# Performance work log

Hardware: AMD Instinct MI355X
Metric: run time of the kernel (lower is better)

Reference implementation:

```python
import jax, jax.numpy as jnp
import numpy as np
from jax import lax

NUM_HEADS = 8
EPS = 1e-12  # torch F.normalize eps


def setup_inputs() -> dict:
    key = jax.random.key(0)
    ks = jax.random.split(key, 5)
    dim = 192
    b, h, w = 8, 128, 128
    return {
        "x": jax.random.normal(ks[0], (b, dim, h, w), jnp.float32),
        "w_qkv": jax.random.normal(ks[1], (3 * dim, dim, 1, 1), jnp.float32) * (1.0 / np.sqrt(dim)),
        "w_dw": jax.random.normal(ks[2], (3 * dim, 1, 3, 3), jnp.float32) * (1.0 / 3.0),
        "w_proj": jax.random.normal(ks[3], (dim, dim, 1, 1), jnp.float32) * (1.0 / np.sqrt(dim)),
        "temperature": jnp.ones((NUM_HEADS, 1, 1), jnp.float32),
    }


def _l2norm(t):
    n = jnp.sqrt(jnp.sum(t * t, axis=-1, keepdims=True))
    return t / jnp.maximum(n, EPS)


def reference(x, w_qkv, w_dw, w_proj, temperature):
    b, c, h, w = x.shape
    # 1x1 conv to 3*dim channels
    qkv = jnp.einsum('bchw,oc->bohw', x, w_qkv[:, :, 0, 0])
    # depthwise 3x3 conv, dilation=2, padding=2, groups=3*dim
    qkv = lax.conv_general_dilated(
        qkv, w_dw, window_strides=(1, 1), padding=((2, 2), (2, 2)),
        rhs_dilation=(2, 2), feature_group_count=3 * c,
        dimension_numbers=('NCHW', 'OIHW', 'NCHW'))
    q, k, v = jnp.split(qkv, 3, axis=1)
    ch = c // NUM_HEADS
    def heads(t):  # b (head ch) h w -> b head ch (h w)
        return t.reshape(b, NUM_HEADS, ch, h * w)
    q, k, v = heads(q), heads(k), heads(v)
    q = _l2norm(q)
    k = _l2norm(k)
    attn = jnp.einsum('bhcn,bhdn->bhcd', q, k) * temperature  # (b, head, ch, ch)
    attn = jax.nn.softmax(attn, axis=-1)
    out = jnp.einsum('bhcd,bhdn->bhcn', attn, v)
    out = out.reshape(b, c, h, w)
    out = jnp.einsum('bchw,oc->bohw', out, w_proj[:, :, 0, 0])
    return out
```

## Files before the change

### kernel.cpp

```cpp
#include <hip/hip_runtime.h>


#define DIM 192
#define NH 8
#define CH 24
#define IH 128
#define IW 128
#define NPIX (IH*IW)
#define BATCH 8
#define QKVC (3*DIM)
#define PAD 200
#define TPAD 136
#define SPAD 264

typedef unsigned short u16;
typedef short bf16x8 __attribute__((ext_vector_type(8)));
typedef float f32x4 __attribute__((ext_vector_type(4)));

__device__ __forceinline__ float b2f(u16 u){
    unsigned v = ((unsigned)u) << 16;
    return __builtin_bit_cast(float, v);
}
__device__ __forceinline__ u16 f2b(float f){
    unsigned u = __builtin_bit_cast(unsigned, f);
    u += 0x7fffu + ((u >> 16) & 1u);
    return (u16)(u >> 16);
}

__device__ __forceinline__ void conv_row8(const u16* __restrict__ rp, int px0,
        float w0, float w1, float w2, float* o_){
    float f[12];
    if(px0 > 0){
        unsigned u = *(const unsigned*)(rp + px0 - 2);
        f[0] = b2f((u16)u); f[1] = b2f((u16)(u >> 16));
    } else { f[0] = 0.f; f[1] = 0.f; }
    bf16x8 v = *(const bf16x8*)(rp + px0);
    #pragma unroll
    for(int j=0;j<8;j++) f[2+j] = b2f((u16)v[j]);
    if(px0 < 120){
        unsigned u = *(const unsigned*)(rp + px0 + 8);
        f[10] = b2f((u16)u); f[11] = b2f((u16)(u >> 16));
    } else { f[10] = 0.f; f[11] = 0.f; }
    #pragma unroll
    for(int i=0;i<8;i++) o_[i] += w0*f[i] + w1*f[i+2] + w2*f[i+4];
}

__global__ __launch_bounds__(256) void k1_qkv(const float* __restrict__ x,
        const float* __restrict__ wqkv, u16* __restrict__ qkv_pre){
    __shared__ __align__(16) u16 Xl[128*PAD];
    __shared__ __align__(16) u16 Wl[64*PAD];
    const int tid = threadIdx.x;
    const int pt = blockIdx.x, b = blockIdx.y;
    const int p0 = pt*128;
    {
        const int px = tid & 127, half = tid >> 7;
        const float* xb = x + (size_t)b*DIM*NPIX + p0 + px;
        for(int cg = 0; cg < 12; cg++){
            int cb = half*96 + cg*8;
            bf16x8 v;
            #pragma unroll
            for(int j=0;j<8;j++) v[j] = (short)f2b(xb[(size_t)(cb+j)*NPIX]);
            *(bf16x8*)&Xl[px*PAD + cb] = v;
        }
    }
    const int lane = tid & 63, w = tid >> 6;
    const int r = lane & 15, quad = lane >> 4;
    const int mbase = (w & 1)*32, nbase = (w >> 1)*64;
    u16* Tl = Wl;
    for(int ot = 0; ot < 9; ot++){
        const int obase = ot*64;
        for(int i = tid; i < 64*24; i += 256){
            int o = i/24, k8 = (i%24)*8;
            const float* wp = wqkv + (size_t)(obase+o)*DIM + k8;
            bf16x8 v;
            #pragma unroll
            for(int j=0;j<8;j++) v[j] = (short)f2b(wp[j]);
            *(bf16x8*)&Wl[o*PAD + k8] = v;
        }
        __syncthreads();
        f32x4 acc[8];
        { f32x4 z = {0.f,0.f,0.f,0.f}; for(int i=0;i<8;i++) acc[i]=z; }
        #pragma unroll
        for(int kk = 0; kk < 6; kk++){
            const int k0 = kk*32 + quad*8;
            bf16x8 a0 = *(const bf16x8*)&Wl[(mbase + r)*PAD + k0];
            bf16x8 a1 = *(const bf16x8*)&Wl[(mbase + 16 + r)*PAD + k0];
            #pragma unroll
            for(int ni=0; ni<4; ni++){
                bf16x8 bb = *(const bf16x8*)&Xl[(nbase + ni*16 + r)*PAD + k0];
                acc[ni*2+0] = __builtin_amdgcn_mfma_f32_16x16x32_bf16(a0, bb, acc[ni*2+0], 0,0,0);
                acc[ni*2+1] = __builtin_amdgcn_mfma_f32_16x16x32_bf16(a1, bb, acc[ni*2+1], 0,0,0);
            }
        }
        __syncthreads();
        #pragma unroll
        for(int ni=0; ni<4; ni++)
            #pragma unroll
            for(int mi=0; mi<2; mi++){
                int o_loc = mbase + mi*16 + quad*4;
                int p_loc = nbase + ni*16 + r;
                #pragma unroll
                for(int t=0;t<4;t++)
                    Tl[(o_loc+t)*TPAD + p_loc] = f2b(acc[ni*2+mi][t]);
            }
        __syncthreads();
        u16* op = qkv_pre + ((size_t)b*QKVC + obase)*NPIX + p0;
        for(int it = 0; it < 4; it++){
            int idx = tid + it*256;
            int o = idx >> 4, oct = idx & 15;
            bf16x8 v = *(const bf16x8*)&Tl[o*TPAD + oct*8];
            *(bf16x8*)&op[(size_t)o*NPIX + oct*8] = v;
        }
        __syncthreads();
    }
}

__global__ __launch_bounds__(256) void k2_gram(const u16* __restrict__ qkv_pre,
        const float* __restrict__ wdw, float* __restrict__ G){
    __shared__ __align__(16) u16 Sl[48*SPAD];
    const int tid = threadIdx.x;
    const int pc = blockIdx.x, h = blockIdx.y, b = blockIdx.z;
    const int lane = tid & 63, w = tid >> 6;
    const int r = lane & 15, quad = lane >> 4;
    f32x4 acc[6];
    { f32x4 z = {0.f,0.f,0.f,0.f}; for(int i=0;i<6;i++) acc[i]=z; }
    for(int chunk = 0; chunk < 2; chunk++){
        if(chunk) __syncthreads();
        for(int it = 0; it < 6; it++){
            int t = tid + it*256;
            int c48 = t >> 5, oct = t & 31;
            int isK = (c48 >= CH);
            int c = isK ? (c48 - CH) : c48;
            int ch = (isK ? DIM : 0) + h*CH + c;
            const u16* base = qkv_pre + ((size_t)b*QKVC + ch)*NPIX;
            const float* wv = wdw + ch*9;
            int py = pc*4 + chunk*2 + (oct >> 4);
            int px0 = (oct & 15)*8;
            float o_[8];
            #pragma unroll
            for(int i=0;i<8;i++) o_[i]=0.f;
            #pragma unroll
            for(int ky=0;ky<3;ky++){
                int ry = py + 2*ky - 2;
                if(ry < 0 || ry >= IH) continue;
                conv_row8(base + ry*IW, px0, wv[ky*3], wv[ky*3+1], wv[ky*3+2], o_);
            }
            bf16x8 v;
            #pragma unroll
            for(int i=0;i<8;i++) v[i] = (short)f2b(o_[i]);
            *(bf16x8*)&Sl[c48*SPAD + oct*8] = v;
        }
        __syncthreads();
        #pragma unroll
        for(int kk = 0; kk < 2; kk++){
            const int k0 = w*64 + kk*32 + quad*8;
            bf16x8 f0 = *(const bf16x8*)&Sl[(     r)*SPAD + k0];
            bf16x8 f1 = *(const bf16x8*)&Sl[(16 + r)*SPAD + k0];
            bf16x8 f2 = *(const bf16x8*)&Sl[(32 + r)*SPAD + k0];
            acc[0] = __builtin_amdgcn_mfma_f32_16x16x32_bf16(f0, f0, acc[0], 0,0,0);
            acc[1] = __builtin_amdgcn_mfma_f32_16x16x32_bf16(f0, f1, acc[1], 0,0,0);
            acc[2] = __builtin_amdgcn_mfma_f32_16x16x32_bf16(f0, f2, acc[2], 0,0,0);
            acc[3] = __builtin_amdgcn_mfma_f32_16x16x32_bf16(f1, f1, acc[3], 0,0,0);
            acc[4] = __builtin_amdgcn_mfma_f32_16x16x32_bf16(f1, f2, acc[4], 0,0,0);
            acc[5] = __builtin_amdgcn_mfma_f32_16x16x32_bf16(f2, f2, acc[5], 0,0,0);
        }
    }
    __syncthreads();
    float* R = (float*)Sl;
    #pragma unroll
    for(int tile=0; tile<6; tile++)
        *(f32x4*)&R[(w*6 + tile)*256 + lane*4] = acc[tile];
    __syncthreads();
    float* Gb = G + (size_t)(b*NH + h)*48*48;
    #pragma unroll
    for(int i=0; i<6; i++){
        int idx = tid + i*256;
        int tile = idx >> 8, rem = idx & 255;
        int ln = rem >> 2, t = rem & 3;
        float s = R[idx] + R[1536 + idx] + R[2*1536 + idx] + R[3*1536 + idx];
        int ti = (tile<3) ? 0 : ((tile<5) ? 1 : 2);
        int tj = (tile<3) ? tile : ((tile<5) ? (tile-2) : 2);
        int c = ti*16 + (ln >> 4)*4 + t;
        int d = tj*16 + (ln & 15);
        atomicAdd(&Gb[c*48 + d], s);
    }
}

__global__ __launch_bounds__(256) void k4_vconv(u16* __restrict__ qkv_pre,
        const float* __restrict__ wdw){
    const int tid = threadIdx.x;
    const int oct = tid & 15, pyl = tid >> 4;
    const int band = blockIdx.x, cp = blockIdx.y, b = blockIdx.z;
    const int py = band*16 + pyl, px0 = oct*8;
    #pragma unroll
    for(int j=0;j<2;j++){
        int ch = cp*2 + j;
        const u16* base = qkv_pre + ((size_t)b*QKVC + 2*DIM + ch)*NPIX;
        const float* wv = wdw + (2*DIM + ch)*9;
        float o_[8];
        #pragma unroll
        for(int i=0;i<8;i++) o_[i]=0.f;
        #pragma unroll
        for(int ky=0;ky<3;ky++){
            int ry = py + 2*ky - 2;
            if(ry < 0 || ry >= IH) continue;
            conv_row8(base + ry*IW, px0, wv[ky*3], wv[ky*3+1], wv[ky*3+2], o_);
        }
        bf16x8 v;
        #pragma unroll
        for(int i=0;i<8;i++) v[i] = (short)f2b(o_[i]);
        *(bf16x8*)&qkv_pre[((size_t)b*QKVC + ch)*NPIX + py*IW + px0] = v;
    }
}

__global__ __launch_bounds__(256) void k3_attn(const float* __restrict__ G,
        const float* __restrict__ temp, const float* __restrict__ wproj,
        float* __restrict__ M){
    __shared__ float attn[NH][CH][CH];
    __shared__ float nq[DIM], nk[DIM];
    const int b = blockIdx.x, tid = threadIdx.x;
    const float* Gb = G + (size_t)b*NH*48*48;
    if(tid < DIM){
        int h = tid / CH, c = tid % CH;
        const float* g = Gb + (size_t)h*48*48;
        nq[tid] = fmaxf(sqrtf(g[c*48 + c]), 1e-12f);
        nk[tid] = fmaxf(sqrtf(g[(CH+c)*48 + (CH+c)]), 1e-12f);
    }
    __syncthreads();
    if(tid < DIM){
        int h = tid / CH, c = tid % CH;
        float t = temp[h];
        const float* g = Gb + (size_t)h*48*48 + c*48 + CH;
        float row[CH];
        float mx = -1e30f;
        #pragma unroll
        for(int d=0; d<CH; d++){
            float v = g[d] / (nq[tid]*nk[h*CH+d]) * t;
            row[d]=v; mx = fmaxf(mx,v);
        }
        float sum=0.f;
        #pragma unroll
        for(int d=0;d<CH;d++){ row[d]=expf(row[d]-mx); sum+=row[d]; }
        float inv = 1.f/sum;
        #pragma unroll
        for(int d=0;d<CH;d++) attn[h][c][d] = row[d]*inv;
    }
    __syncthreads();
    float* Mb = M + (size_t)b*DIM*DIM;
    for(int i = tid; i < DIM*DIM; i += 256){
        int o = i / DIM, hd = i % DIM;
        int h = hd / CH, d = hd % CH;
        float s = 0.f;
        #pragma unroll
        for(int c=0;c<CH;c++)
            s += wproj[o*DIM + h*CH + c] * attn[h][c][d];
        Mb[i] = s;
    }
}

__global__ __launch_bounds__(256) void k5_out(const u16* __restrict__ qkv_pre,
        const float* __restrict__ M, float* __restrict__ out){
    __shared__ __align__(16) u16 vl[128*PAD];
    __shared__ __align__(16) u16 Ml[64*PAD];
    const int tid = threadIdx.x;
    const int py = blockIdx.x, b = blockIdx.y;
    const int p0 = py*IW;
    {
        const int px = tid & 127, half = tid >> 7;
        const u16* vb = qkv_pre + (size_t)b*QKVC*NPIX + p0 + px;
        for(int cg = 0; cg < 12; cg++){
            int cb = half*96 + cg*8;
            bf16x8 v;
            #pragma unroll
            for(int j=0;j<8;j++) v[j] = (short)vb[(size_t)(cb+j)*NPIX];
            *(bf16x8*)&vl[px*PAD + cb] = v;
        }
    }
    const int lane = tid & 63, w = tid >> 6;
    const int r = lane & 15, quad = lane >> 4;
    const int mbase = (w & 1)*32, nbase = (w >> 1)*64;
    for(int ot = 0; ot < 3; ot++){
        const int obase = ot*64;
        for(int i = tid; i < 64*24; i += 256){
            int o = i/24, k8 = (i%24)*8;
            const float* mp = M + ((size_t)b*DIM + obase + o)*DIM + k8;
            bf16x8 v;
            #pragma unroll
            for(int j=0;j<8;j++) v[j] = (short)f2b(mp[j]);
            *(bf16x8*)&Ml[o*PAD + k8] = v;
        }
        __syncthreads();
        f32x4 acc[8];
        { f32x4 z = {0.f,0.f,0.f,0.f}; for(int i=0;i<8;i++) acc[i]=z; }
        #pragma unroll
        for(int kk = 0; kk < 6; kk++){
            const int k0 = kk*32 + quad*8;
            bf16x8 a0 = *(const bf16x8*)&Ml[(mbase + r)*PAD + k0];
            bf16x8 a1 = *(const bf16x8*)&Ml[(mbase + 16 + r)*PAD + k0];
            #pragma unroll
            for(int ni=0; ni<4; ni++){
                bf16x8 bb = *(const bf16x8*)&vl[(nbase + ni*16 + r)*PAD + k0];
                acc[ni*2+0] = __builtin_amdgcn_mfma_f32_16x16x32_bf16(a0, bb, acc[ni*2+0], 0,0,0);
                acc[ni*2+1] = __builtin_amdgcn_mfma_f32_16x16x32_bf16(a1, bb, acc[ni*2+1], 0,0,0);
            }
        }
        float* op = out + ((size_t)b*DIM + obase)*NPIX + p0;
        #pragma unroll
        for(int ni=0; ni<4; ni++)
            #pragma unroll
            for(int mi=0; mi<2; mi++){
                int o_loc = mbase + mi*16 + quad*4;
                int p_loc = nbase + ni*16 + r;
                #pragma unroll
                for(int t=0;t<4;t++)
                    op[(size_t)(o_loc+t)*NPIX + p_loc] = acc[ni*2+mi][t];
            }
        __syncthreads();
    }
}

extern "C" void kernel_launch(void* const* d_in, const int* in_sizes, int n_in,
                              void* d_out, int out_size, void* d_ws, size_t ws_size,
                              hipStream_t stream){
    const float* x     = (const float*)d_in[0];
    const float* wqkv  = (const float*)d_in[1];
    const float* wdw   = (const float*)d_in[2];
    const float* wproj = (const float*)d_in[3];
    const float* temp  = (const float*)d_in[4];
    float* out = (float*)d_out;

    char* ws = (char*)d_ws;
    u16* qkv_pre = (u16*)ws;
    size_t off = (size_t)BATCH*QKVC*NPIX*sizeof(u16);
    float* G   = (float*)(ws + off); off += (size_t)BATCH*NH*48*48*4;
    float* M   = (float*)(ws + off); off += (size_t)BATCH*DIM*DIM*4;

    hipMemsetAsync(G, 0, (size_t)BATCH*NH*48*48*sizeof(float), stream);

    k1_qkv <<<dim3(128, BATCH), 256, 0, stream>>>(x, wqkv, qkv_pre);
    k2_gram<<<dim3(32, NH, BATCH), 256, 0, stream>>>(qkv_pre, wdw, G);
    k4_vconv<<<dim3(8, 96, BATCH), 256, 0, stream>>>(qkv_pre, wdw);
    k3_attn<<<BATCH, 256, 0, stream>>>(G, temp, wproj, M);
    k5_out <<<dim3(128, BATCH), 256, 0, stream>>>(qkv_pre, M, out);
}
```

Before: 447.1 us.

## Pre-convert weights to bf16 and read MFMA A operands directly from global

Adds a small kernel that converts the qkv weight to bf16 once, and makes the attention kernel emit the fused projection matrix M in bf16. The k1 and k5 GEMM kernels then load weight fragments straight from global/L2 instead of staging them through shared memory each tile, which removes several __syncthreads per output tile and the per-block fp32-to-bf16 conversion. k1 also swaps the MFMA operand order so each lane holds four consecutive pixels, letting it store packed bf16 results directly to global without the LDS transpose. The costs are scattered global loads for the A operands and narrower 8-byte stores, plus one extra kernel launch.

```diff
diff --git a/kernel.cpp b/kernel.cpp
--- a/kernel.cpp
+++ b/kernel.cpp
@@ -10,7 +10,6 @@
 #define BATCH 8
 #define QKVC (3*DIM)
 #define PAD 200
-#define TPAD 136
 #define SPAD 264
 
 typedef unsigned short u16;
@@ -45,10 +44,18 @@
     for(int i=0;i<8;i++) o_[i] += w0*f[i] + w1*f[i+2] + w2*f[i+4];
 }
 
+__global__ __launch_bounds__(256) void k0_wcvt(const float* __restrict__ wqkv,
+        u16* __restrict__ wb){
+    int i = (blockIdx.x*256 + threadIdx.x)*4;
+    f32x4 v = *(const f32x4*)&wqkv[i];
+    unsigned lo = ((unsigned)f2b(v[1]) << 16) | f2b(v[0]);
+    unsigned hi = ((unsigned)f2b(v[3]) << 16) | f2b(v[2]);
+    *(uint2*)&wb[i] = make_uint2(lo, hi);
+}
+
 __global__ __launch_bounds__(256) void k1_qkv(const float* __restrict__ x,
-        const float* __restrict__ wqkv, u16* __restrict__ qkv_pre){
+        const u16* __restrict__ wb, u16* __restrict__ qkv_pre){
     __shared__ __align__(16) u16 Xl[128*PAD];
-    __shared__ __align__(16) u16 Wl[64*PAD];
     const int tid = threadIdx.x;
     const int pt = blockIdx.x, b = blockIdx.y;
     const int p0 = pt*128;
@@ -63,55 +70,40 @@
             *(bf16x8*)&Xl[px*PAD + cb] = v;
         }
     }
+    __syncthreads();
     const int lane = tid & 63, w = tid >> 6;
     const int r = lane & 15, quad = lane >> 4;
     const int mbase = (w & 1)*32, nbase = (w >> 1)*64;
-    u16* Tl = Wl;
+    u16* op = qkv_pre + (size_t)b*QKVC*NPIX + p0;
     for(int ot = 0; ot < 9; ot++){
         const int obase = ot*64;
-        for(int i = tid; i < 64*24; i += 256){
-            int o = i/24, k8 = (i%24)*8;
-            const float* wp = wqkv + (size_t)(obase+o)*DIM + k8;
-            bf16x8 v;
-            #pragma unroll
-            for(int j=0;j<8;j++) v[j] = (short)f2b(wp[j]);
-            *(bf16x8*)&Wl[o*PAD + k8] = v;
-        }
-        __syncthreads();
         f32x4 acc[8];
         { f32x4 z = {0.f,0.f,0.f,0.f}; for(int i=0;i<8;i++) acc[i]=z; }
+        const u16* w0p = wb + (size_t)(obase + mbase + r)*DIM;
+        const u16* w1p = w0p + 16*DIM;
         #pragma unroll
         for(int kk = 0; kk < 6; kk++){
             const int k0 = kk*32 + quad*8;
-            bf16x8 a0 = *(const bf16x8*)&Wl[(mbase + r)*PAD + k0];
-            bf16x8 a1 = *(const bf16x8*)&Wl[(mbase + 16 + r)*PAD + k0];
+            bf16x8 a0 = *(const bf16x8*)&w0p[k0];
+            bf16x8 a1 = *(const bf16x8*)&w1p[k0];
             #pragma unroll
             for(int ni=0; ni<4; ni++){
                 bf16x8 bb = *(const bf16x8*)&Xl[(nbase + ni*16 + r)*PAD + k0];
-                acc[ni*2+0] = __builtin_amdgcn_mfma_f32_16x16x32_bf16(a0, bb, acc[ni*2+0], 0,0,0);
-                acc[ni*2+1] = __builtin_amdgcn_mfma_f32_16x16x32_bf16(a1, bb, acc[ni*2+1], 0,0,0);
-            }
-        }
-        __syncthreads();
+                acc[ni*2+0] = __builtin_amdgcn_mfma_f32_16x16x32_bf16(bb, a0, acc[ni*2+0], 0,0,0);
+                acc[ni*2+1] = __builtin_amdgcn_mfma_f32_16x16x32_bf16(bb, a1, acc[ni*2+1], 0,0,0);
+            }
+        }
         #pragma unroll
         for(int ni=0; ni<4; ni++)
             #pragma unroll
             for(int mi=0; mi<2; mi++){
-                int o_loc = mbase + mi*16 + quad*4;
-                int p_loc = nbase + ni*16 + r;
-                #pragma unroll
-                for(int t=0;t<4;t++)
-                    Tl[(o_loc+t)*TPAD + p_loc] = f2b(acc[ni*2+mi][t]);
-            }
-        __syncthreads();
-        u16* op = qkv_pre + ((size_t)b*QKVC + obase)*NPIX + p0;
-        for(int it = 0; it < 4; it++){
-            int idx = tid + it*256;
-            int o = idx >> 4, oct = idx & 15;
-            bf16x8 v = *(const bf16x8*)&Tl[o*TPAD + oct*8];
-            *(bf16x8*)&op[(size_t)o*NPIX + oct*8] = v;
-        }
-        __syncthreads();
+                int o = obase + mbase + mi*16 + r;
+                int px = nbase + ni*16 + quad*4;
+                f32x4 a = acc[ni*2+mi];
+                unsigned lo = ((unsigned)f2b(a[1]) << 16) | f2b(a[0]);
+                unsigned hi = ((unsigned)f2b(a[3]) << 16) | f2b(a[2]);
+                *(uint2*)&op[(size_t)o*NPIX + px] = make_uint2(lo, hi);
+            }
     }
 }
 
@@ -215,7 +207,7 @@
 
 __global__ __launch_bounds__(256) void k3_attn(const float* __restrict__ G,
         const float* __restrict__ temp, const float* __restrict__ wproj,
-        float* __restrict__ M){
+        u16* __restrict__ M){
     __shared__ float attn[NH][CH][CH];
     __shared__ float nq[DIM], nk[DIM];
     const int b = blockIdx.x, tid = threadIdx.x;
@@ -246,7 +238,7 @@
         for(int d=0;d<CH;d++) attn[h][c][d] = row[d]*inv;
     }
     __syncthreads();
-    float* Mb = M + (size_t)b*DIM*DIM;
+    u16* Mb = M + (size_t)b*DIM*DIM;
     for(int i = tid; i < DIM*DIM; i += 256){
         int o = i / DIM, hd = i % DIM;
         int h = hd / CH, d = hd % CH;
@@ -254,14 +246,13 @@
         #pragma unroll
         for(int c=0;c<CH;c++)
             s += wproj[o*DIM + h*CH + c] * attn[h][c][d];
-        Mb[i] = s;
+        Mb[i] = f2b(s);
     }
 }
 
 __global__ __launch_bounds__(256) void k5_out(const u16* __restrict__ qkv_pre,
-        const float* __restrict__ M, float* __restrict__ out){
+        const u16* __restrict__ M, float* __restrict__ out){
     __shared__ __align__(16) u16 vl[128*PAD];
-    __shared__ __align__(16) u16 Ml[64*PAD];
     const int tid = threadIdx.x;
     const int py = blockIdx.x, b = blockIdx.y;
     const int p0 = py*IW;
@@ -276,27 +267,22 @@
             *(bf16x8*)&vl[px*PAD + cb] = v;
         }
     }
+    __syncthreads();
     const int lane = tid & 63, w = tid >> 6;
     const int r = lane & 15, quad = lane >> 4;
     const int mbase = (w & 1)*32, nbase = (w >> 1)*64;
+    const u16* Mb = M + (size_t)b*DIM*DIM;
     for(int ot = 0; ot < 3; ot++){
         const int obase = ot*64;
-        for(int i = tid; i < 64*24; i += 256){
-            int o = i/24, k8 = (i%24)*8;
-            const float* mp = M + ((size_t)b*DIM + obase + o)*DIM + k8;
-            bf16x8 v;
-            #pragma unroll
-            for(int j=0;j<8;j++) v[j] = (short)f2b(mp[j]);
-            *(bf16x8*)&Ml[o*PAD + k8] = v;
-        }
-        __syncthreads();
         f32x4 acc[8];
         { f32x4 z = {0.f,0.f,0.f,0.f}; for(int i=0;i<8;i++) acc[i]=z; }
+        const u16* m0 = Mb + (size_t)(obase + mbase + r)*DIM;
+        const u16* m1 = m0 + 16*DIM;
         #pragma unroll
         for(int kk = 0; kk < 6; kk++){
             const int k0 = kk*32 + quad*8;
-            bf16x8 a0 = *(const bf16x8*)&Ml[(mbase + r)*PAD + k0];
-            bf16x8 a1 = *(const bf16x8*)&Ml[(mbase + 16 + r)*PAD + k0];
+            bf16x8 a0 = *(const bf16x8*)&m0[k0];
+            bf16x8 a1 = *(const bf16x8*)&m1[k0];
             #pragma unroll
             for(int ni=0; ni<4; ni++){
                 bf16x8 bb = *(const bf16x8*)&vl[(nbase + ni*16 + r)*PAD + k0];
@@ -315,7 +301,6 @@
                 for(int t=0;t<4;t++)
                     op[(size_t)(o_loc+t)*NPIX + p_loc] = acc[ni*2+mi][t];
             }
-        __syncthreads();
     }
 }
 
@@ -332,12 +317,14 @@
     char* ws = (char*)d_ws;
     u16* qkv_pre = (u16*)ws;
     size_t off = (size_t)BATCH*QKVC*NPIX*sizeof(u16);
-    float* G   = (float*)(ws + off); off += (size_t)BATCH*NH*48*48*4;
-    float* M   = (float*)(ws + off); off += (size_t)BATCH*DIM*DIM*4;
+    float* G  = (float*)(ws + off); off += (size_t)BATCH*NH*48*48*4;
+    u16* M    = (u16*)(ws + off);   off += (size_t)BATCH*DIM*DIM*2;
+    u16* wb   = (u16*)(ws + off);   off += (size_t)QKVC*DIM*2;
 
     hipMemsetAsync(G, 0, (size_t)BATCH*NH*48*48*sizeof(float), stream);
 
-    k1_qkv <<<dim3(128, BATCH), 256, 0, stream>>>(x, wqkv, qkv_pre);
+    k0_wcvt<<<108, 256, 0, stream>>>(wqkv, wb);
+    k1_qkv <<<dim3(128, BATCH), 256, 0, stream>>>(x, wb, qkv_pre);
     k2_gram<<<dim3(32, NH, BATCH), 256, 0, stream>>>(qkv_pre, wdw, G);
     k4_vconv<<<dim3(8, 96, BATCH), 256, 0, stream>>>(qkv_pre, wdw);
     k3_attn<<<BATCH, 256, 0, stream>>>(G, temp, wproj, M);
```

Result: faster. 433.8 us (-3.0%).
